# Kernel optimization log

Hardware: AMD Instinct MI355X
Metric: run time of the kernel (lower is better)

## Reference

```python
import jax, jax.numpy as jnp
import numpy as np
import jax.scipy.linalg as jsl

# dims
B, DIN = 4096, 256      # data
OUT, M = 32, 128        # output GPs, inducing points
NH = 2                  # hyperparameter samples
JITTER = 1e-4


def vec2tril(vec, m):
    """Fill lower-triangular (row-major) from packed vector."""
    i, j = jnp.tril_indices(m)
    out = jnp.zeros(vec.shape[:-1] + (m, m), vec.dtype)
    return out.at[..., i, j].set(vec)


def _hypers(theta):
    sf2 = jnp.exp(theta[:, 0])        # (NH,) signal variance
    ls = jnp.exp(theta[:, 1:])        # (NH, DIN) ARD lengthscales
    return sf2, ls


def kernel_zz(theta, z):
    """RBF K(z,z): (NH, OUT, M, M)."""
    sf2, ls = _hypers(theta)
    zs = z[None] / ls[:, None, None, :]              # (NH, OUT, M, DIN)
    n2 = (zs ** 2).sum(-1)                           # (NH, OUT, M)
    cross = jnp.einsum('homd,hond->homn', zs, zs)
    d2 = jnp.maximum(n2[..., :, None] + n2[..., None, :] - 2.0 * cross, 0.0)
    return sf2[:, None, None, None] * jnp.exp(-0.5 * d2)


def kernel_zx(theta, z, x):
    """RBF K(z,x): (NH, OUT, M, B)."""
    sf2, ls = _hypers(theta)
    zs = z[None] / ls[:, None, None, :]              # (NH, OUT, M, DIN)
    xs = x[None] / ls[:, None, :]                    # (NH, B, DIN)
    z2 = (zs ** 2).sum(-1)                           # (NH, OUT, M)
    x2 = (xs ** 2).sum(-1)                           # (NH, B)
    cross = jnp.einsum('homd,hbd->homb', zs, xs)     # (NH, OUT, M, B)
    d2 = jnp.maximum(z2[..., None] + x2[:, None, None, :] - 2.0 * cross, 0.0)
    return sf2[:, None, None, None] * jnp.exp(-0.5 * d2)


def setup_inputs() -> dict:
    key = jax.random.key(0)
    k1, k2, k3, k4, k5 = jax.random.split(key, 5)
    x = jax.random.normal(k1, (B, DIN), jnp.float32)
    z = jax.random.normal(k2, (OUT, M, DIN), jnp.float32)
    u_mean = jax.random.normal(k3, (OUT, M, 1), jnp.float32) * 0.5
    u_tril_vec = jax.random.uniform(k4, (OUT, M * (M + 1) // 2), jnp.float32)
    theta = jax.random.normal(k5, (NH, 1 + DIN), jnp.float32)
    return {"x": x, "z": z, "u_mean": u_mean, "u_tril_vec": u_tril_vec, "theta": theta}


def reference(x, z, u_mean, u_tril_vec, theta):
    m = z.shape[-2]
    u_tril = vec2tril(u_tril_vec, m)                        # (OUT, M, M)

    kuf = kernel_zx(theta, z, x)                            # (NH, OUT, M, B)
    kuu = kernel_zz(theta, z)                               # (NH, OUT, M, M)
    Lkuu = jnp.linalg.cholesky(kuu + JITTER * jnp.eye(m, dtype=kuu.dtype))

    bshape = Lkuu.shape[:-2]
    u_mean_b = jnp.broadcast_to(u_mean, bshape + u_mean.shape[-2:])
    u_tril_b = jnp.broadcast_to(u_tril, bshape + u_tril.shape[-2:])

    LKinvu = jsl.solve_triangular(Lkuu, u_mean_b, lower=True)   # (NH, OUT, M, 1)
    LKinvKuf = jsl.solve_triangular(Lkuu, kuf, lower=True)      # (NH, OUT, M, B)

    sf2, _ = _hypers(theta)
    kff_diag = sf2[:, None, None]                               # (NH, 1, 1)

    diag1 = (LKinvKuf ** 2).sum(-2)                             # (NH, OUT, B)
    LKinvLs = jsl.solve_triangular(Lkuu, u_tril_b, lower=True)  # (NH, OUT, M, M)
    vec2 = jnp.einsum('...ij,...ik->...jk', LKinvLs, LKinvKuf)  # (NH, OUT, M, B)
    diag2 = (vec2 ** 2).sum(-2)                                 # (NH, OUT, B)

    mu = jnp.einsum('...ij,...ik->...jk', LKinvKuf, LKinvu)[..., 0]  # (NH, OUT, B)
    var = kff_diag - diag1 + diag2                                   # (NH, OUT, B)
    return mu, var
```

## Files before the change

### kernel.cpp

```cpp
#include <hip/hip_runtime.h>
#include <cstdint>
#include <cstddef>

constexpr int B_   = 4096;
constexpr int DIN  = 256;
constexpr int OUT_ = 32;
constexpr int MM   = 128;
constexpr int NH_  = 2;
constexpr int HO   = 64;
constexpr int TRIL = 8256;
constexpr float JIT = 1e-4f;

constexpr size_t al4k(size_t x){ return (x + 4095) & ~size_t(4095); }
constexpr size_t OFF_FLAG  = 0;
constexpr size_t OFF_INVLS = 4096;
constexpr size_t OFF_SF2   = al4k(OFF_INVLS + 2*256*4);
constexpr size_t OFF_ZN2   = al4k(OFF_SF2 + 64);
constexpr size_t OFF_XN2   = al4k(OFF_ZN2 + 8192*4);
constexpr size_t OFF_W     = al4k(OFF_XN2 + 8192*4);
constexpr size_t OFF_ZS    = al4k(OFF_W + 8192*4);
constexpr size_t OFF_XS    = al4k(OFF_ZS + (size_t)2097152*2);
constexpr size_t OFF_VTH   = al4k(OFF_XS + (size_t)2097152*2);
constexpr size_t OFF_VTL   = al4k(OFF_VTH + (size_t)1048576*2);
constexpr size_t OFF_CHI   = al4k(OFF_VTL + (size_t)1048576*2);
constexpr size_t OFF_CLO   = al4k(OFF_CHI + (size_t)1048576*2);

typedef float f32x4 __attribute__((ext_vector_type(4)));
typedef short short8 __attribute__((ext_vector_type(8)));

__device__ __forceinline__ float bf2f(unsigned short u){
  union{unsigned int i; float f;} v; v.i = ((unsigned)u) << 16; return v.f;
}
__device__ __forceinline__ unsigned short f2bf(float f){
  union{float f; unsigned int i;} v; v.f = f;
  unsigned int r = v.i + 0x7fffu + ((v.i >> 16) & 1u);
  return (unsigned short)(r >> 16);
}
__device__ __forceinline__ float ldin(const void* p, size_t i, int isbf){
  if (isbf) return bf2f(((const unsigned short*)p)[i]);
  return ((const float*)p)[i];
}
__device__ __forceinline__ void stout(void* p, size_t i, float v, int isbf){
  if (isbf) ((unsigned short*)p)[i] = f2bf(v);
  else ((float*)p)[i] = v;
}
__device__ __forceinline__ void gl_lds16(const unsigned short* g, unsigned short* l){
  __builtin_amdgcn_global_load_lds(
      (const __attribute__((address_space(1))) unsigned int*)g,
      (__attribute__((address_space(3))) unsigned int*)l, 16, 0, 0);
}

__global__ void k_hypers(const void* __restrict__ theta, const void* __restrict__ x,
                         int* __restrict__ flagp,
                         float* __restrict__ inv_ls, float* __restrict__ sf2){
  __shared__ int sflag;
  int t = threadIdx.x;
  if (t < 64){
    unsigned int w0 = ((const unsigned int*)theta)[t];
    unsigned int w1 = ((const unsigned int*)x)[t];
    float a0 = fabsf(bf2f((unsigned short)(w0 & 0xffffu)));
    float a1 = fabsf(bf2f((unsigned short)(w1 & 0xffffu)));
    int c = ((a0 > 9.3e-10f && a0 < 64.f) ? 1 : 0) + ((a1 > 9.3e-10f && a1 < 64.f) ? 1 : 0);
    c += __shfl_down(c, 32); c += __shfl_down(c, 16); c += __shfl_down(c, 8);
    c += __shfl_down(c, 4);  c += __shfl_down(c, 2);  c += __shfl_down(c, 1);
    if (t == 0){ sflag = (c >= 64) ? 1 : 0; *flagp = sflag; }
  }
  __syncthreads();
  const int isbf = sflag;
  for (int i = t; i < NH_*257; i += blockDim.x){
    int h = i / 257, j = i - h*257;
    float v = ldin(theta, i, isbf);
    if (j == 0) sf2[h] = __expf(v);
    else inv_ls[h*DIN + j - 1] = __expf(-v);
  }
}

__global__ void k_scale(const void* __restrict__ xsrc, const void* __restrict__ zsrc,
                        const int* flagp, const float* __restrict__ inv_ls,
                        unsigned short* __restrict__ xdst, unsigned short* __restrict__ zdst,
                        float* __restrict__ xn2, float* __restrict__ zn2){
  const int isbf = *flagp;
  const int wave = threadIdx.x >> 6, lane = threadIdx.x & 63;
  int bx = blockIdx.x;
  const void* src; unsigned short* dst; float* n2; int r;
  if (bx < 1024){ src = xsrc; dst = xdst; n2 = xn2; r = bx*4 + wave; }
  else          { src = zsrc; dst = zdst; n2 = zn2; r = (bx-1024)*4 + wave; }
  const int d0 = lane*4;
  float v[4];
  if (isbf){
    uint2 uu = *(const uint2*)((const unsigned short*)src + (size_t)r*DIN + d0);
    v[0]=bf2f((unsigned short)(uu.x & 0xffffu)); v[1]=bf2f((unsigned short)(uu.x >> 16));
    v[2]=bf2f((unsigned short)(uu.y & 0xffffu)); v[3]=bf2f((unsigned short)(uu.y >> 16));
  } else {
    f32x4 f = *(const f32x4*)((const float*)src + (size_t)r*DIN + d0);
    v[0]=f[0]; v[1]=f[1]; v[2]=f[2]; v[3]=f[3];
  }
  #pragma unroll
  for (int h = 0; h < 2; ++h){
    f32x4 il = *(const f32x4*)(inv_ls + h*DIN + d0);
    unsigned short rb[4];
    float p = 0.f;
    #pragma unroll
    for (int k = 0; k < 4; ++k){
      float s = v[k] * il[k];
      rb[k] = f2bf(s);
      float qv = bf2f(rb[k]);
      p += qv*qv;
    }
    uint2 pk;
    pk.x = (unsigned)rb[0] | ((unsigned)rb[1] << 16);
    pk.y = (unsigned)rb[2] | ((unsigned)rb[3] << 16);
    *(uint2*)(dst + ((size_t)h*4096 + r)*DIN + d0) = pk;
    p += __shfl_xor(p, 32); p += __shfl_xor(p, 16); p += __shfl_xor(p, 8);
    p += __shfl_xor(p, 4);  p += __shfl_xor(p, 2);  p += __shfl_xor(p, 1);
    if (lane == 0) n2[(size_t)h*4096 + r] = p;
  }
}

constexpr int TLD = 20;
constexpr int TSZ = 16*TLD;
__device__ __forceinline__ int tb(int bi, int bj){ return (bi*(bi+1)/2 + bj)*TSZ; }
__device__ __forceinline__ int vb(int bi, int bj){ return (36 + bi*(bi-1)/2 + bj)*TSZ; }
__device__ __forceinline__ int tri_bi(int t){
  int bi = (int)((sqrtf(8.f*t + 1.f) - 1.f) * 0.5f);
  while ((bi+1)*(bi+2)/2 <= t) ++bi;
  while (bi*(bi+1)/2 > t) --bi;
  return bi;
}

__global__ __launch_bounds__(512) void k_fact(
    const unsigned short* __restrict__ zs, const float* __restrict__ zn2,
    const float* __restrict__ sf2,
    const void* __restrict__ u_mean, const void* __restrict__ u_tril,
    const int* flagp, float* __restrict__ wg,
    unsigned short* __restrict__ Chi, unsigned short* __restrict__ Clo){
  const int ho = blockIdx.x, h = ho >> 5, o = ho & 31;
  const int tid = threadIdx.x;
  const int lane = tid & 63, wid = tid >> 6;
  const int l15 = lane & 15, q = lane >> 4;
  const int wn = wid * 16;
  const int isbf = *flagp;
  extern __shared__ char smem[];
  float* T = (float*)smem;
  float* zn2l = T + 64*TSZ;
  unsigned short* zsl = (unsigned short*)T;
  unsigned short* VTh = (unsigned short*)(smem + 82432);
  unsigned short* VTl = (unsigned short*)(smem + 117248);
  unsigned short* Sth = (unsigned short*)smem;
  unsigned short* Stl = (unsigned short*)(smem + 34816);
  unsigned short* Qh = VTh;
  unsigned short* Ql = VTl;
  float* ul    = (float*)(smem + 152064);
  float* wpart = (float*)(smem + 152576);

  if (tid < 128){
    zn2l[tid] = zn2[ho*128 + tid];
    ul[tid]   = ldin(u_mean, (size_t)o*128 + tid, isbf);
  }
  const size_t zbase = (size_t)ho * 32768;
  const int sw = ((q ^ ((l15 >> 1) & 3)) << 3);
  const int rA = wn + (lane >> 2);
  const int sg = ((lane & 3) ^ ((rA >> 1) & 3)) << 3;
  const f32x4 z4 = {0.f,0.f,0.f,0.f};
  f32x4 acck[8];
  #pragma unroll
  for (int mt=0; mt<8; ++mt) acck[mt]=z4;
  for (int kc = 0; kc < 8; ++kc){
    __syncthreads();
    gl_lds16(zs + zbase + (size_t)rA*256 + kc*32 + sg, zsl + wn*32);
    __syncthreads();
    short8 b0 = *(const short8*)(zsl + (wn + l15)*32 + sw);
    #pragma unroll
    for (int mt=0; mt<8; ++mt){
      short8 a = *(const short8*)(zsl + (mt*16 + l15)*32 + sw);
      acck[mt] = __builtin_amdgcn_mfma_f32_16x16x32_bf16(a, b0, acck[mt], 0,0,0);
    }
  }
  __syncthreads();
  const float s2v = sf2[h];
  {
    const int n = wn + l15;
    const float nn = zn2l[n];
    const int bn = wid;
    #pragma unroll
    for (int mt=0; mt<8; ++mt){
      #pragma unroll
      for (int r=0; r<4; ++r){
        int m = mt*16 + q*4 + r;
        float d2 = fmaxf(zn2l[m] + nn - 2.f*acck[mt][r], 0.f);
        float a = s2v * __expf(-0.5f*d2);
        if (m == n) a += JIT;
        int bm = m >> 4;
        if (bn <= bm) T[tb(bm, bn) + (m & 15)*TLD + (n & 15)] = a;
      }
    }
  }
  __syncthreads();
  for (int kb = 0; kb < 8; ++kb){
    if (wid == 0){
      float* D = T + tb(kb, kb);
      const int r = lane & 15;
      const bool act = (lane < 16);
      float a[16];
      #pragma unroll
      for (int k = 0; k < 16; ++k) a[k] = 0.f;
      if (act){
        #pragma unroll
        for (int k2 = 0; k2 < 4; ++k2)
          *(f32x4*)(a + 4*k2) = *(const f32x4*)(D + r*TLD + 4*k2);
      }
      #pragma unroll
      for (int c = 0; c < 16; ++c){
        float pr[16];
        #pragma unroll
        for (int k = 0; k < 16; ++k) pr[k] = __shfl(a[k], c);
        float rsq = rsqrtf(pr[c]);
        if (act && r >= c) a[c] *= rsq;
        float lrc = a[c];
        #pragma unroll
        for (int k = 0; k < 16; ++k)
          if (k > c && act && r > c) a[k] -= lrc * (pr[k] * rsq);
      }
      float v[16];
      #pragma unroll
      for (int k = 0; k < 16; ++k) v[k] = 0.f;
      const int c = lane & 15;
      #pragma unroll
      for (int i = 0; i < 16; ++i){
        float lrow[16];
        #pragma unroll
        for (int k = 0; k < 16; ++k) lrow[k] = __shfl(a[k], i);
        float rli = 1.f / lrow[i];
        float s = 0.f;
        #pragma unroll
        for (int k = 0; k < 16; ++k)
          if (k < i) s += ((k >= c) ? lrow[k]*v[k] : 0.f);
        v[i] = (c == i) ? rli : ((c < i) ? -s*rli : 0.f);
      }
      if (act){
        #pragma unroll
        for (int i = 0; i < 16; ++i) D[i*TLD + c] = v[i];
      }
    }
    __syncthreads();
    {
      const int gi = kb*16 + 16 + tid;
      if (gi < 128){
        float* Bp = T + tb(gi >> 4, kb) + (gi & 15)*TLD;
        const float* Vd = T + tb(kb, kb);
        float b[16], nb[16];
        #pragma unroll
        for (int k2 = 0; k2 < 4; ++k2) *(f32x4*)(b + 4*k2) = *(const f32x4*)(Bp + 4*k2);
        #pragma unroll
        for (int j = 0; j < 16; ++j){
          float s = 0.f;
          #pragma unroll
          for (int k = 0; k < 16; ++k)
            if (k <= j) s += b[k] * Vd[j*TLD + k];
          nb[j] = s;
        }
        #pragma unroll
        for (int k2 = 0; k2 < 4; ++k2) *(f32x4*)(Bp + 4*k2) = *(const f32x4*)(nb + 4*k2);
      }
    }
    __syncthreads();
    {
      const int D8 = 7 - kb;
      const int Tn = D8*(D8+1)/2;
      const int r15 = lane & 15, c0 = (lane >> 4)*4;
      for (int tt = wid; tt < Tn; tt += 8){
        int bi1 = tri_bi(tt);
        int bj1 = tt - bi1*(bi1+1)/2;
        int bi = kb + 1 + bi1, bj = kb + 1 + bj1;
        const float* Lr = T + tb(bi, kb) + r15*TLD;
        const float* Lc = T + tb(bj, kb) + c0*TLD;
        float* Cp = T + tb(bi, bj) + r15*TLD + c0;
        float lr[16];
        #pragma unroll
        for (int k2 = 0; k2 < 4; ++k2) *(f32x4*)(lr + 4*k2) = *(const f32x4*)(Lr + 4*k2);
        f32x4 accv = *(const f32x4*)Cp;
        #pragma unroll
        for (int cc = 0; cc < 4; ++cc){
          float lc[16];
          #pragma unroll
          for (int k2 = 0; k2 < 4; ++k2) *(f32x4*)(lc + 4*k2) = *(const f32x4*)(Lc + cc*TLD + 4*k2);
          float s = 0.f;
          #pragma unroll
          for (int k = 0; k < 16; ++k) s += lr[k]*lc[k];
          accv[cc] -= s;
        }
        *(f32x4*)Cp = accv;
      }
    }
    __syncthreads();
  }
  {
    const int r15 = lane & 15, c0 = (lane >> 4)*4;
    for (int d = 1; d < 8; ++d){
      for (int tt = wid; tt < 8 - d; tt += 8){
        const int bi = d + tt, jb = bi - d;
        float W0=0.f, W1=0.f, W2=0.f, W3=0.f;
        for (int k = jb; k < bi; ++k){
          const float* Lt = T + tb(bi, k) + r15*TLD;
          const float* Vt = (k == jb) ? (T + tb(jb, jb)) : (T + vb(k, jb));
          float lr[16];
          #pragma unroll
          for (int k2 = 0; k2 < 4; ++k2) *(f32x4*)(lr + 4*k2) = *(const f32x4*)(Lt + 4*k2);
          #pragma unroll
          for (int kk = 0; kk < 16; ++kk){
            f32x4 vv = *(const f32x4*)(Vt + kk*TLD + c0);
            W0 += lr[kk]*vv[0]; W1 += lr[kk]*vv[1];
            W2 += lr[kk]*vv[2]; W3 += lr[kk]*vv[3];
          }
        }
        const float* Vd = T + tb(bi, bi) + r15*TLD;
        const int cgl = (lane >> 4);
        f32x4 Rr = {0.f,0.f,0.f,0.f};
        #pragma unroll
        for (int k = 0; k < 16; ++k){
          float vd = Vd[k];
          float w0 = __shfl(W0, (cgl<<4)|k);
          float w1 = __shfl(W1, (cgl<<4)|k);
          float w2 = __shfl(W2, (cgl<<4)|k);
          float w3 = __shfl(W3, (cgl<<4)|k);
          Rr[0] -= vd*w0; Rr[1] -= vd*w1; Rr[2] -= vd*w2; Rr[3] -= vd*w3;
        }
        *(f32x4*)(T + vb(bi, jb) + r15*TLD + c0) = Rr;
      }
      __syncthreads();
    }
  }
  for (int e = tid; e < 16384; e += 512){
    int c = e >> 7, rr = e & 127;
    int bc = c >> 4, br = rr >> 4;
    float v = 0.f;
    if (br == bc)      v = T[tb(br, bc) + (rr & 15)*TLD + (c & 15)];
    else if (br > bc)  v = T[vb(br, bc) + (rr & 15)*TLD + (c & 15)];
    unsigned short hi = f2bf(v);
    VTh[c*136 + rr] = hi;
    VTl[c*136 + rr] = f2bf(v - bf2f(hi));
  }
  __syncthreads();
  f32x4 acc[8];
  #pragma unroll
  for (int mt=0; mt<8; ++mt) acc[mt]=z4;
  #pragma unroll
  for (int kc2 = 0; kc2 < 4; ++kc2){
    const int ko = kc2*32 + q*8;
    short8 b0h = *(const short8*)(VTh + (wn + l15)*136 + ko);
    short8 b0l = *(const short8*)(VTl + (wn + l15)*136 + ko);
    #pragma unroll
    for (int mt=0; mt<8; ++mt){
      short8 ah = *(const short8*)(VTh + (mt*16 + l15)*136 + ko);
      short8 al = *(const short8*)(VTl + (mt*16 + l15)*136 + ko);
      acc[mt] = __builtin_amdgcn_mfma_f32_16x16x32_bf16(ah, b0h, acc[mt], 0,0,0);
      acc[mt] = __builtin_amdgcn_mfma_f32_16x16x32_bf16(ah, b0l, acc[mt], 0,0,0);
      acc[mt] = __builtin_amdgcn_mfma_f32_16x16x32_bf16(al, b0h, acc[mt], 0,0,0);
    }
  }
  {
    float u0 = ul[wn + l15];
    float wpm[32];
    #pragma unroll
    for (int mt=0; mt<8; ++mt){
      #pragma unroll
      for (int r=0; r<4; ++r)
        wpm[mt*4+r] = acc[mt][r]*u0;
    }
    #pragma unroll
    for (int i = 0; i < 32; ++i){
      wpm[i] += __shfl_xor(wpm[i], 1);
      wpm[i] += __shfl_xor(wpm[i], 2);
      wpm[i] += __shfl_xor(wpm[i], 4);
      wpm[i] += __shfl_xor(wpm[i], 8);
    }
    if (l15 == 0){
      #pragma unroll
      for (int i = 0; i < 32; ++i){
        int m = (i>>2)*16 + q*4 + (i&3);
        wpart[wid*128 + m] = wpm[i];
      }
    }
  }
  __syncthreads();
  if (tid < 128){
    float s = 0.f;
    #pragma unroll
    for (int wv = 0; wv < 8; ++wv) s += wpart[wv*128 + tid];
    wg[ho*128 + tid] = s;
  }
  {
    const int n0 = wn + l15;
    #pragma unroll
    for (int mt=0; mt<8; ++mt){
      #pragma unroll
      for (int r=0; r<4; ++r){
        int m = mt*16 + q*4 + r;
        float v0 = acc[mt][r];
        unsigned short h0 = f2bf(v0);
        Qh[m*136 + n0] = h0; Ql[m*136 + n0] = f2bf(v0 - bf2f(h0));
      }
    }
  }
  for (int e = tid; e < 16384; e += 512){
    int k = e >> 7, j = e & 127;
    float val = 0.f;
    if (j <= k) val = ldin(u_tril, (size_t)o*TRIL + (size_t)k*(k+1)/2 + j, isbf);
    unsigned short hi = f2bf(val);
    Sth[j*136 + k] = hi;
    Stl[j*136 + k] = f2bf(val - bf2f(hi));
  }
  __syncthreads();
  f32x4 acc3[8];
  #pragma unroll
  for (int mt=0; mt<8; ++mt) acc3[mt]=z4;
  #pragma unroll
  for (int kc2 = 0; kc2 < 4; ++kc2){
    const int ko = kc2*32 + q*8;
    short8 b0h = *(const short8*)(Sth + (wn + l15)*136 + ko);
    short8 b0l = *(const short8*)(Stl + (wn + l15)*136 + ko);
    #pragma unroll
    for (int mt=0; mt<8; ++mt){
      short8 ah = *(const short8*)(Qh + (mt*16 + l15)*136 + ko);
      short8 al = *(const short8*)(Ql + (mt*16 + l15)*136 + ko);
      acc3[mt] = __builtin_amdgcn_mfma_f32_16x16x32_bf16(ah, b0h, acc3[mt], 0,0,0);
      acc3[mt] = __builtin_amdgcn_mfma_f32_16x16x32_bf16(al, b0h, acc3[mt], 0,0,0);
      acc3[mt] = __builtin_amdgcn_mfma_f32_16x16x32_bf16(ah, b0l, acc3[mt], 0,0,0);
    }
  }
  __syncthreads();
  {
    const int n0 = wn + l15;
    #pragma unroll
    for (int mt=0; mt<8; ++mt){
      #pragma unroll
      for (int r=0; r<4; ++r){
        int m = mt*16 + q*4 + r;
        float v0 = acc3[mt][r];
        unsigned short h0 = f2bf(v0);
        Qh[m*136 + n0] = h0; Ql[m*136 + n0] = f2bf(v0 - bf2f(h0));
      }
    }
  }
  __syncthreads();
  f32x4 acc2[8];
  #pragma unroll
  for (int mt=0; mt<8; ++mt) acc2[mt]=z4;
  #pragma unroll
  for (int kc2 = 0; kc2 < 4; ++kc2){
    const int ko = kc2*32 + q*8;
    short8 b0h = *(const short8*)(Qh + (wn + l15)*136 + ko);
    short8 b0l = *(const short8*)(Ql + (wn + l15)*136 + ko);
    #pragma unroll
    for (int mt=0; mt<8; ++mt){
      short8 ah = *(const short8*)(Qh + (mt*16 + l15)*136 + ko);
      short8 al = *(const short8*)(Ql + (mt*16 + l15)*136 + ko);
      acc2[mt] = __builtin_amdgcn_mfma_f32_16x16x32_bf16(ah, b0h, acc2[mt], 0,0,0);
      acc2[mt] = __builtin_amdgcn_mfma_f32_16x16x32_bf16(ah, b0l, acc2[mt], 0,0,0);
      acc2[mt] = __builtin_amdgcn_mfma_f32_16x16x32_bf16(al, b0h, acc2[mt], 0,0,0);
    }
  }
  {
    const size_t vbase = (size_t)ho * 16384;
    const int n = wn + l15;
    #pragma unroll
    for (int mt=0; mt<8; ++mt){
      #pragma unroll
      for (int r=0; r<4; ++r){
        int m = mt*16 + q*4 + r;
        float c = acc[mt][r] - acc2[mt][r];
        unsigned short hi = f2bf(c);
        unsigned short lo = f2bf(c - bf2f(hi));
        Chi[vbase + m*128 + n] = hi;
        Clo[vbase + m*128 + n] = lo;
      }
    }
  }
}

__global__ __launch_bounds__(256, 2) void k_main(
    const unsigned short* __restrict__ zs, const unsigned short* __restrict__ xs,
    const float* __restrict__ zn2, const float* __restrict__ xn2,
    const float* __restrict__ wg, const unsigned short* __restrict__ Chi,
    const unsigned short* __restrict__ Clo, const float* __restrict__ sf2,
    const int* flagp, void* __restrict__ out){
  const int bblk = blockIdx.x, ho = blockIdx.y, h = ho >> 5;
  const int tid = threadIdx.x;
  const int lane = tid & 63, l15 = lane & 15, q = lane >> 4;
  const int wid = tid >> 6;
  const int wn = wid * 32;
  const int wn2 = wid * 64;
  const int isbf = *flagp;
  extern __shared__ char smem[];
  unsigned short* zb0 = (unsigned short*)smem;
  unsigned short* zb1 = zb0 + 4096;
  unsigned short* zb2 = zb0 + 8192;
  unsigned short* kufT = (unsigned short*)smem;
  float* zn2l = (float*)(smem + 69632);
  float* xn2l = zn2l + 128;
  float* wl   = xn2l + 256;

  if (tid < 128){
    zn2l[tid] = zn2[ho*128 + tid];
    wl[tid]   = wg[ho*128 + tid];
  }
  xn2l[tid] = xn2[(size_t)h*B_ + bblk*256 + tid];
  const size_t zbase = (size_t)ho * 32768;
  const size_t xbase = ((size_t)h*B_ + bblk*256) * 256;
  const int sw = ((q ^ ((l15 >> 1) & 3)) << 3);
  const int rA = wn + (lane >> 2);
  const int sg = ((lane & 3) ^ ((rA >> 1) & 3)) << 3;
  const f32x4 z4 = {0.f,0.f,0.f,0.f};
  f32x4 acc[8][4];
  #pragma unroll
  for (int mt=0; mt<8; ++mt){
    #pragma unroll
    for (int nt=0; nt<4; ++nt) acc[mt][nt]=z4;
  }
  unsigned short* zbp[3] = { zb0, zb1, zb2 };

  auto STAGEZ = [&](int c, unsigned short* zd){
    const int off = c*32;
    gl_lds16(zs + zbase + (size_t)rA*256      + off + sg, zd + wn*32);
    gl_lds16(zs + zbase + (size_t)(rA+16)*256 + off + sg, zd + (wn+16)*32);
  };
  auto LDB = [&](int c, short8* bd){
    #pragma unroll
    for (int nt=0; nt<4; ++nt)
      bd[nt] = *(const short8*)(xs + xbase + (size_t)(wn2 + nt*16 + l15)*256 + c*32 + q*8);
  };

  short8 bA[4], bB[4];
  STAGEZ(0, zb0);
  STAGEZ(1, zb1);
  LDB(0, bA);

  #pragma unroll
  for (int kc = 0; kc < 8; ++kc){
    unsigned short* zc = zbp[kc % 3];
    if (kc + 2 < 8) STAGEZ(kc + 2, zbp[(kc + 2) % 3]);
    if (kc + 1 < 8){ if (kc & 1) LDB(kc + 1, bA); else LDB(kc + 1, bB); }
    if (kc < 6)       asm volatile("s_waitcnt vmcnt(6)" ::: "memory");
    else if (kc == 6) asm volatile("s_waitcnt vmcnt(4)" ::: "memory");
    else              asm volatile("s_waitcnt vmcnt(0)" ::: "memory");
    __builtin_amdgcn_s_barrier();
    __builtin_amdgcn_sched_barrier(0);
    const short8* bc = (kc & 1) ? bB : bA;
    #pragma unroll
    for (int mt=0; mt<8; ++mt){
      short8 a = *(const short8*)(zc + (mt*16 + l15)*32 + sw);
      #pragma unroll
      for (int nt=0; nt<4; ++nt)
        acc[mt][nt] = __builtin_amdgcn_mfma_f32_16x16x32_bf16(a, bc[nt], acc[mt][nt], 0,0,0);
    }
    asm volatile("s_waitcnt lgkmcnt(0)" ::: "memory");
    __builtin_amdgcn_sched_barrier(0);
    __builtin_amdgcn_s_barrier();
  }
  const float s2 = sf2[h];
  float mu[4] = {0.f, 0.f, 0.f, 0.f};
  #pragma unroll
  for (int nt=0; nt<4; ++nt){
    const int bl = wn2 + nt*16 + l15;
    const float xn = xn2l[bl];
    #pragma unroll
    for (int mt=0; mt<8; ++mt){
      const int m0 = mt*16 + q*4;
      float kf[4];
      #pragma unroll
      for (int r=0; r<4; ++r){
        float d2 = fmaxf(zn2l[m0+r] + xn - 2.f*acc[mt][nt][r], 0.f);
        kf[r] = s2 * __expf(-0.5f*d2);
        mu[nt] += wl[m0+r] * kf[r];
      }
      uint2 pk;
      pk.x = (unsigned)f2bf(kf[0]) | ((unsigned)f2bf(kf[1]) << 16);
      pk.y = (unsigned)f2bf(kf[2]) | ((unsigned)f2bf(kf[3]) << 16);
      *(uint2*)(kufT + (size_t)bl*136 + m0) = pk;
    }
  }
  __syncthreads();
  f32x4 acc2[8][4];
  #pragma unroll
  for (int mt=0; mt<8; ++mt){
    #pragma unroll
    for (int nt=0; nt<4; ++nt) acc2[mt][nt]=z4;
  }
  const unsigned short* Ch = Chi + (size_t)ho*16384;
  const unsigned short* Cl = Clo + (size_t)ho*16384;
  #pragma unroll
  for (int kc2 = 0; kc2 < 4; ++kc2){
    short8 bk[4];
    #pragma unroll
    for (int nt=0; nt<4; ++nt)
      bk[nt] = *(const short8*)(kufT + (wn2 + nt*16 + l15)*136 + kc2*32 + q*8);
    #pragma unroll
    for (int mt=0; mt<8; ++mt){
      short8 ah = *(const short8*)(Ch + (mt*16 + l15)*128 + kc2*32 + q*8);
      short8 al = *(const short8*)(Cl + (mt*16 + l15)*128 + kc2*32 + q*8);
      #pragma unroll
      for (int nt=0; nt<4; ++nt){
        acc2[mt][nt] = __builtin_amdgcn_mfma_f32_16x16x32_bf16(ah, bk[nt], acc2[mt][nt], 0,0,0);
        acc2[mt][nt] = __builtin_amdgcn_mfma_f32_16x16x32_bf16(al, bk[nt], acc2[mt][nt], 0,0,0);
      }
    }
  }
  float s2p[4] = {0.f, 0.f, 0.f, 0.f};
  #pragma unroll
  for (int nt=0; nt<4; ++nt){
    const int bl = wn2 + nt*16 + l15;
    #pragma unroll
    for (int mt=0; mt<8; ++mt){
      const int m0 = mt*16 + q*4;
      uint2 pk = *(const uint2*)(kufT + (size_t)bl*136 + m0);
      f32x4 t = acc2[mt][nt];
      s2p[nt] += bf2f((unsigned short)(pk.x & 0xffff)) * t[0]
               + bf2f((unsigned short)(pk.x >> 16))    * t[1]
               + bf2f((unsigned short)(pk.y & 0xffff)) * t[2]
               + bf2f((unsigned short)(pk.y >> 16))    * t[3];
    }
  }
  #pragma unroll
  for (int nt=0; nt<4; ++nt){
    mu[nt]  += __shfl_xor(mu[nt], 16);  mu[nt]  += __shfl_xor(mu[nt], 32);
    s2p[nt] += __shfl_xor(s2p[nt], 16); s2p[nt] += __shfl_xor(s2p[nt], 32);
  }
  if (lane < 16){
    #pragma unroll
    for (int nt=0; nt<4; ++nt){
      size_t col = (size_t)ho*B_ + bblk*256 + wn2 + nt*16 + lane;
      stout(out, col,                  mu[nt],        isbf);
      stout(out, (size_t)HO*B_ + col,  s2 - s2p[nt],  isbf);
    }
  }
}

extern "C" void kernel_launch(void* const* d_in, const int* in_sizes, int n_in,
                              void* d_out, int out_size, void* d_ws, size_t ws_size,
                              hipStream_t stream) {
  const void* x      = d_in[0];
  const void* z      = d_in[1];
  const void* u_mean = d_in[2];
  const void* u_tril = d_in[3];
  const void* theta  = d_in[4];
  char* ws = (char*)d_ws;

  int*   flag   = (int*)(ws + OFF_FLAG);
  float* inv_ls = (float*)(ws + OFF_INVLS);
  float* sf2    = (float*)(ws + OFF_SF2);
  float* zn2    = (float*)(ws + OFF_ZN2);
  float* xn2    = (float*)(ws + OFF_XN2);
  float* wv     = (float*)(ws + OFF_W);
  unsigned short* zsw = (unsigned short*)(ws + OFF_ZS);
  unsigned short* xsw = (unsigned short*)(ws + OFF_XS);
  unsigned short* Chi = (unsigned short*)(ws + OFF_CHI);
  unsigned short* Clo = (unsigned short*)(ws + OFF_CLO);

  k_hypers<<<1, 256, 0, stream>>>(theta, x, flag, inv_ls, sf2);
  k_scale<<<dim3(2048), 256, 0, stream>>>(x, z, flag, inv_ls, xsw, zsw, xn2, zn2);
  k_fact<<<64, 512, 156672, stream>>>(zsw, zn2, sf2, u_mean, u_tril, flag, wv, Chi, Clo);
  k_main<<<dim3(16, 64), 256, 69632 + 2048, stream>>>(zsw, xsw, zn2, xn2, wv, Chi, Clo, sf2, flag, (void*)d_out);
}
```

Before: 226.1 us.

## Triple-buffer z staging in k_fact and overlap Cholesky panel with trailing update

The K(z,z) GEMM loop now stages z chunks into three rotating LDS buffers two steps ahead, using explicit vmcnt waits and raw barriers in place of two syncthreads per iteration. The blocked Cholesky is reordered as a lookahead schedule. Wave 7 first updates the next diagonal block, then wave 0 factors it while waves 1-7 apply the remaining trailing updates. This is meant to hide global-load latency and the serial single-wave panel factorisation, at the cost of an extra barrier per step and one fewer wave for trailing updates. Tile index 0 is skipped in the trailing loop (tt starts at wid with stride 7), which relies on tile 0 being the already-updated diagonal block.

Result: slower. 242.7 us (+7.3%).

```diff
diff --git a/kernel.cpp b/kernel.cpp
--- a/kernel.cpp
+++ b/kernel.cpp
@@ -143,7 +143,6 @@
   extern __shared__ char smem[];
   float* T = (float*)smem;
   float* zn2l = T + 64*TSZ;
-  unsigned short* zsl = (unsigned short*)T;
   unsigned short* VTh = (unsigned short*)(smem + 82432);
   unsigned short* VTl = (unsigned short*)(smem + 117248);
   unsigned short* Sth = (unsigned short*)smem;
@@ -152,6 +151,10 @@
   unsigned short* Ql = VTl;
   float* ul    = (float*)(smem + 152064);
   float* wpart = (float*)(smem + 152576);
+  unsigned short* zbB0 = (unsigned short*)(smem + 82432);
+  unsigned short* zbB1 = (unsigned short*)(smem + 90624);
+  unsigned short* zbB2 = (unsigned short*)(smem + 98816);
+  unsigned short* zbB[3] = { zbB0, zbB1, zbB2 };
 
   if (tid < 128){
     zn2l[tid] = zn2[ho*128 + tid];
@@ -162,21 +165,36 @@
   const int rA = wn + (lane >> 2);
   const int sg = ((lane & 3) ^ ((rA >> 1) & 3)) << 3;
   const f32x4 z4 = {0.f,0.f,0.f,0.f};
+
+  auto STAGEZ = [&](int c, unsigned short* zd){
+    gl_lds16(zs + zbase + (size_t)rA*256 + c*32 + sg, zd + wn*32);
+  };
+
   f32x4 acck[8];
   #pragma unroll
   for (int mt=0; mt<8; ++mt) acck[mt]=z4;
+  STAGEZ(0, zbB0);
+  STAGEZ(1, zbB1);
+  __syncthreads();
+  #pragma unroll
   for (int kc = 0; kc < 8; ++kc){
-    __syncthreads();
-    gl_lds16(zs + zbase + (size_t)rA*256 + kc*32 + sg, zsl + wn*32);
-    __syncthreads();
-    short8 b0 = *(const short8*)(zsl + (wn + l15)*32 + sw);
-    #pragma unroll
-    for (int mt=0; mt<8; ++mt){
-      short8 a = *(const short8*)(zsl + (mt*16 + l15)*32 + sw);
+    unsigned short* zc = zbB[kc % 3];
+    if (kc + 2 < 8) STAGEZ(kc + 2, zbB[(kc + 2) % 3]);
+    if (kc < 6)       asm volatile("s_waitcnt vmcnt(2)" ::: "memory");
+    else if (kc == 6) asm volatile("s_waitcnt vmcnt(1)" ::: "memory");
+    else              asm volatile("s_waitcnt vmcnt(0)" ::: "memory");
+    __builtin_amdgcn_s_barrier();
+    __builtin_amdgcn_sched_barrier(0);
+    short8 b0 = *(const short8*)(zc + (wn + l15)*32 + sw);
+    #pragma unroll
+    for (int mt=0; mt<8; ++mt){
+      short8 a = *(const short8*)(zc + (mt*16 + l15)*32 + sw);
       acck[mt] = __builtin_amdgcn_mfma_f32_16x16x32_bf16(a, b0, acck[mt], 0,0,0);
     }
-  }
-  __syncthreads();
+    asm volatile("s_waitcnt lgkmcnt(0)" ::: "memory");
+    __builtin_amdgcn_sched_barrier(0);
+    __builtin_amdgcn_s_barrier();
+  }
   const float s2v = sf2[h];
   {
     const int n = wn + l15;
@@ -196,53 +214,76 @@
     }
   }
   __syncthreads();
-  for (int kb = 0; kb < 8; ++kb){
-    if (wid == 0){
-      float* D = T + tb(kb, kb);
-      const int r = lane & 15;
-      const bool act = (lane < 16);
-      float a[16];
-      #pragma unroll
-      for (int k = 0; k < 16; ++k) a[k] = 0.f;
-      if (act){
-        #pragma unroll
-        for (int k2 = 0; k2 < 4; ++k2)
-          *(f32x4*)(a + 4*k2) = *(const f32x4*)(D + r*TLD + 4*k2);
-      }
-      #pragma unroll
-      for (int c = 0; c < 16; ++c){
-        float pr[16];
-        #pragma unroll
-        for (int k = 0; k < 16; ++k) pr[k] = __shfl(a[k], c);
-        float rsq = rsqrtf(pr[c]);
-        if (act && r >= c) a[c] *= rsq;
-        float lrc = a[c];
-        #pragma unroll
-        for (int k = 0; k < 16; ++k)
-          if (k > c && act && r > c) a[k] -= lrc * (pr[k] * rsq);
-      }
-      float v[16];
-      #pragma unroll
-      for (int k = 0; k < 16; ++k) v[k] = 0.f;
-      const int c = lane & 15;
-      #pragma unroll
-      for (int i = 0; i < 16; ++i){
-        float lrow[16];
-        #pragma unroll
-        for (int k = 0; k < 16; ++k) lrow[k] = __shfl(a[k], i);
-        float rli = 1.f / lrow[i];
-        float s = 0.f;
-        #pragma unroll
-        for (int k = 0; k < 16; ++k)
-          if (k < i) s += ((k >= c) ? lrow[k]*v[k] : 0.f);
-        v[i] = (c == i) ? rli : ((c < i) ? -s*rli : 0.f);
-      }
-      if (act){
-        #pragma unroll
-        for (int i = 0; i < 16; ++i) D[i*TLD + c] = v[i];
-      }
-    }
-    __syncthreads();
+  auto PANEL = [&](int kb){
+    float* D = T + tb(kb, kb);
+    const int r = lane & 15;
+    const bool act = (lane < 16);
+    float a[16];
+    #pragma unroll
+    for (int k = 0; k < 16; ++k) a[k] = 0.f;
+    if (act){
+      #pragma unroll
+      for (int k2 = 0; k2 < 4; ++k2)
+        *(f32x4*)(a + 4*k2) = *(const f32x4*)(D + r*TLD + 4*k2);
+    }
+    #pragma unroll
+    for (int c = 0; c < 16; ++c){
+      float pr[16];
+      #pragma unroll
+      for (int k = 0; k < 16; ++k) pr[k] = __shfl(a[k], c);
+      float rsq = rsqrtf(pr[c]);
+      if (act && r >= c) a[c] *= rsq;
+      float lrc = a[c];
+      #pragma unroll
+      for (int k = 0; k < 16; ++k)
+        if (k > c && act && r > c) a[k] -= lrc * (pr[k] * rsq);
+    }
+    float v[16];
+    #pragma unroll
+    for (int k = 0; k < 16; ++k) v[k] = 0.f;
+    const int c = lane & 15;
+    #pragma unroll
+    for (int i = 0; i < 16; ++i){
+      float lrow[16];
+      #pragma unroll
+      for (int k = 0; k < 16; ++k) lrow[k] = __shfl(a[k], i);
+      float rli = 1.f / lrow[i];
+      float s = 0.f;
+      #pragma unroll
+      for (int k = 0; k < 16; ++k)
+        if (k < i) s += ((k >= c) ? lrow[k]*v[k] : 0.f);
+      v[i] = (c == i) ? rli : ((c < i) ? -s*rli : 0.f);
+    }
+    if (act){
+      #pragma unroll
+      for (int i = 0; i < 16; ++i) D[i*TLD + c] = v[i];
+    }
+  };
+  auto UPDT = [&](int bi, int bj, int kb){
+    const int r15 = lane & 15, c0 = (lane >> 4)*4;
+    const float* Lr = T + tb(bi, kb) + r15*TLD;
+    const float* Lc = T + tb(bj, kb) + c0*TLD;
+    float* Cp = T + tb(bi, bj) + r15*TLD + c0;
+    float lr[16];
+    #pragma unroll
+    for (int k2 = 0; k2 < 4; ++k2) *(f32x4*)(lr + 4*k2) = *(const f32x4*)(Lr + 4*k2);
+    f32x4 accv = *(const f32x4*)Cp;
+    #pragma unroll
+    for (int cc = 0; cc < 4; ++cc){
+      float lc[16];
+      #pragma unroll
+      for (int k2 = 0; k2 < 4; ++k2) *(f32x4*)(lc + 4*k2) = *(const f32x4*)(Lc + cc*TLD + 4*k2);
+      float s = 0.f;
+      #pragma unroll
+      for (int k = 0; k < 16; ++k) s += lr[k]*lc[k];
+      accv[cc] -= s;
+    }
+    *(f32x4*)Cp = accv;
+  };
+
+  if (wid == 0) PANEL(0);
+  __syncthreads();
+  for (int kb = 0; kb < 7; ++kb){
     {
       const int gi = kb*16 + 16 + tid;
       if (gi < 128){
@@ -264,32 +305,19 @@
       }
     }
     __syncthreads();
+    if (wid == 7) UPDT(kb+1, kb+1, kb);
+    __syncthreads();
     {
       const int D8 = 7 - kb;
       const int Tn = D8*(D8+1)/2;
-      const int r15 = lane & 15, c0 = (lane >> 4)*4;
-      for (int tt = wid; tt < Tn; tt += 8){
-        int bi1 = tri_bi(tt);
-        int bj1 = tt - bi1*(bi1+1)/2;
-        int bi = kb + 1 + bi1, bj = kb + 1 + bj1;
-        const float* Lr = T + tb(bi, kb) + r15*TLD;
-        const float* Lc = T + tb(bj, kb) + c0*TLD;
-        float* Cp = T + tb(bi, bj) + r15*TLD + c0;
-        float lr[16];
-        #pragma unroll
-        for (int k2 = 0; k2 < 4; ++k2) *(f32x4*)(lr + 4*k2) = *(const f32x4*)(Lr + 4*k2);
-        f32x4 accv = *(const f32x4*)Cp;
-        #pragma unroll
-        for (int cc = 0; cc < 4; ++cc){
-          float lc[16];
-          #pragma unroll
-          for (int k2 = 0; k2 < 4; ++k2) *(f32x4*)(lc + 4*k2) = *(const f32x4*)(Lc + cc*TLD + 4*k2);
-          float s = 0.f;
-          #pragma unroll
-          for (int k = 0; k < 16; ++k) s += lr[k]*lc[k];
-          accv[cc] -= s;
+      if (wid == 0){
+        PANEL(kb+1);
+      } else {
+        for (int tt = wid; tt < Tn; tt += 7){
+          int bi1 = tri_bi(tt);
+          int bj1 = tt - bi1*(bi1+1)/2;
+          UPDT(kb+1+bi1, kb+1+bj1, kb);
         }
-        *(f32x4*)Cp = accv;
       }
     }
     __syncthreads();
```
